# Kernel tuning notes

Measured on AMD Instinct MI355X. Metric: run time of the kernel, lower is better.

Reference implementation:

```python
import jax, jax.numpy as jnp
import numpy as np
from math import sqrt

N_PATCHES = 128
ATTENTION_WINDOW = 10
NEG_FILL = -10000.0


def _mask(L):
    # pid[i] = patch index of position i; channels = L // n_patches
    channels = L // N_PATCHES
    pid = jnp.repeat(jnp.arange(N_PATCHES), channels)
    diff = pid[None, :] - pid[:, None]  # diff[i, j] = pid[j] - pid[i]
    return (diff <= 0) | (diff >= ATTENTION_WINDOW)  # True = masked


def setup_inputs() -> dict:
    key = jax.random.key(0)
    k1, k2, k3 = jax.random.split(key, 3)
    B, H, L, D = 4, 8, 2048, 64
    return {
        "queries": jax.random.normal(k1, (B, H, L, D), dtype=jnp.float32),
        "keys": jax.random.normal(k2, (B, H, L, D), dtype=jnp.float32),
        "values": jax.random.normal(k3, (B, H, L, D), dtype=jnp.float32),
        "log_scale": jnp.asarray(np.log(2.0), dtype=jnp.float32),
    }


def reference(queries, keys, values, log_scale):
    B, H, L, D = queries.shape
    scores = jnp.einsum("bhqd,bhkd->bhqk", queries, keys)
    scale = jnp.clip(jnp.exp(log_scale), 1.0, 30.0) / sqrt(D)
    cmask = _mask(L)[None, None]  # [1,1,L,L]
    pos = jnp.where(cmask, NEG_FILL, scores)
    neg = jnp.where(cmask, NEG_FILL, -scores)
    A = jax.nn.softmax(scale * pos, axis=-1) - jax.nn.softmax(scale * neg, axis=-1)
    return jnp.einsum("bhqk,bhkd->bhqd", A, values)
```

## Files before the change

### kernel.cpp

```cpp
#include <hip/hip_runtime.h>
#include <hip/hip_bf16.h>


#define LSEQ   2048
#define DIM    64
#define CH     16
#define WIN    9
#define GRP    8
#define VCOLS  272

#define SK 72
#define SV 280
#define SA 168
#define UNELEMS 21504

typedef __attribute__((ext_vector_type(8))) short bf16x8;
typedef __attribute__((ext_vector_type(4))) float f32x4;

union BF8 { bf16x8 v; unsigned int u[4]; };

__device__ __forceinline__ unsigned int bfpack(float a, float b) {
  unsigned int ua = (__float_as_uint(a) + 0x8000u) >> 16;
  unsigned int ub = (__float_as_uint(b) + 0x8000u) & 0xFFFF0000u;
  return ua | ub;
}

__device__ __forceinline__ bf16x8 pack8(float4 a, float4 b) {
  BF8 r;
  r.u[0] = bfpack(a.x, a.y);
  r.u[1] = bfpack(a.z, a.w);
  r.u[2] = bfpack(b.x, b.y);
  r.u[3] = bfpack(b.z, b.w);
  return r.v;
}

__global__ __launch_bounds__(512, 4)
void signed_attn_kernel(const float* __restrict__ Q,
                        const float* __restrict__ K,
                        const float* __restrict__ V,
                        const float* __restrict__ LS,
                        float* __restrict__ O) {
  __shared__ __align__(16) unsigned short Vt[DIM * SV];
  __shared__ __align__(16) unsigned short Un[UNELEMS];

  const int g  = blockIdx.x & 15;
  const int bh = blockIdx.x >> 4;
  const int t  = threadIdx.x;
  const int p0 = g * GRP;

  const int kbp = (127 - p0) < 16 ? (127 - p0) : 16;
  const int kb  = kbp * CH;

  const float4* Kg = (const float4*)(K + ((size_t)bh * LSEQ + (size_t)(p0 + 1) * CH) * DIM);
  const float4* Vg = (const float4*)(V + ((size_t)bh * LSEQ + (size_t)(p0 + 1) * CH) * DIM);

  for (int e = t; e < kb * 16; e += 512) {
    int row = e >> 4, d4 = e & 15;
    float4 v = Kg[e];
    *(uint2*)&Un[row * SK + d4 * 4] = make_uint2(bfpack(v.x, v.y), bfpack(v.z, v.w));
  }
  {
    const int nq = kb >> 2;
    for (int e = t; e < nq * 16; e += 512) {
      int cq = e >> 4, d4 = e & 15;
      int c = cq << 2;
      float4 v0 = Vg[(c + 0) * 16 + d4];
      float4 v1 = Vg[(c + 1) * 16 + d4];
      float4 v2 = Vg[(c + 2) * 16 + d4];
      float4 v3 = Vg[(c + 3) * 16 + d4];
      int db = d4 << 2;
      *(uint2*)&Vt[(db + 0) * SV + c] = make_uint2(bfpack(v0.x, v1.x), bfpack(v2.x, v3.x));
      *(uint2*)&Vt[(db + 1) * SV + c] = make_uint2(bfpack(v0.y, v1.y), bfpack(v2.y, v3.y));
      *(uint2*)&Vt[(db + 2) * SV + c] = make_uint2(bfpack(v0.z, v1.z), bfpack(v2.z, v3.z));
      *(uint2*)&Vt[(db + 3) * SV + c] = make_uint2(bfpack(v0.w, v1.w), bfpack(v2.w, v3.w));
    }
  }
  for (int c = kb + (t >> 6); c < VCOLS; c += 8) Vt[(t & 63) * SV + c] = 0;

  const int w  = t >> 6;
  const int l  = t & 63;
  const int lr = l & 15;
  const int q4 = l >> 4;

  const int p   = p0 + w;
  const int npk = (127 - p) < WIN ? (127 - p) : WIN;

  const float* Qg = Q + ((size_t)bh * LSEQ + (size_t)p * CH) * DIM;
  bf16x8 qa[2];
#pragma unroll
  for (int s = 0; s < 2; s++) {
    const float* qp = Qg + lr * DIM + q4 * 8 + 32 * s;
    qa[s] = pack8(*(const float4*)qp, *(const float4*)(qp + 4));
  }

  const float scale = fminf(30.f, fmaxf(1.f, __expf(LS[0]))) * 0.125f;
  const int koff = w * CH;

  __syncthreads();

  f32x4 sacc[WIN];
#pragma unroll
  for (int tl = 0; tl < WIN; tl++) {
    f32x4 acc = {0.f, 0.f, 0.f, 0.f};
#pragma unroll
    for (int s = 0; s < 2; s++) {
      bf16x8 b = *(const bf16x8*)&Un[(koff + tl * 16 + lr) * SK + q4 * 8 + 32 * s];
      acc = __builtin_amdgcn_mfma_f32_16x16x32_bf16(qa[s], b, acc, 0, 0, 0);
    }
    sacc[tl] = acc;
  }

  __syncthreads();

  unsigned short* Aw = Un + w * 16 * SA;
#pragma unroll
  for (int tl = 0; tl < WIN; tl++) {
    const bool val = tl < npk;
#pragma unroll
    for (int r = 0; r < 4; r++) {
      float e1 = __expf(scale * sacc[tl][r]);
      unsigned int u = (__float_as_uint(e1) + 0x8000u) >> 16;
      Aw[(q4 * 4 + r) * SA + tl * 16 + lr] = (unsigned short)(val ? u : 0u);
    }
  }
#pragma unroll
  for (int r = 0; r < 4; r++)
    Aw[(q4 * 4 + r) * SA + 144 + lr] = 0;

  BF8 bones;
#pragma unroll
  for (int j = 0; j < 4; j++) bones.u[j] = 0x3F803F80u;

  f32x4 o1[4] = {{0,0,0,0},{0,0,0,0},{0,0,0,0},{0,0,0,0}};
  f32x4 o2[4] = {{0,0,0,0},{0,0,0,0},{0,0,0,0},{0,0,0,0}};
  f32x4 s1 = {0,0,0,0}, s2 = {0,0,0,0};

#pragma unroll
  for (int s = 0; s < 5; s++) {
    BF8 a1, a2;
    a1.v = *(const bf16x8*)&Aw[lr * SA + s * 32 + q4 * 8];
#pragma unroll
    for (int j = 0; j < 4; j++) {
      unsigned int d    = a1.u[j];
      unsigned int lo16 = d << 16;
      unsigned int hi16 = d & 0xFFFF0000u;
      float lo = __uint_as_float(lo16);
      float hi = __uint_as_float(hi16);
      float rl = (lo16 == 0u) ? 0.f : __builtin_amdgcn_rcpf(lo);
      float rh = (hi16 == 0u) ? 0.f : __builtin_amdgcn_rcpf(hi);
      a2.u[j] = bfpack(rl, rh);
    }
    s1 = __builtin_amdgcn_mfma_f32_16x16x32_bf16(a1.v, bones.v, s1, 0, 0, 0);
    s2 = __builtin_amdgcn_mfma_f32_16x16x32_bf16(a2.v, bones.v, s2, 0, 0, 0);
#pragma unroll
    for (int n = 0; n < 4; n++) {
      bf16x8 b = *(const bf16x8*)&Vt[(n * 16 + lr) * SV + koff + s * 32 + q4 * 8];
      o1[n] = __builtin_amdgcn_mfma_f32_16x16x32_bf16(a1.v, b, o1[n], 0, 0, 0);
      o2[n] = __builtin_amdgcn_mfma_f32_16x16x32_bf16(a2.v, b, o2[n], 0, 0, 0);
    }
  }

  float* Og = O + ((size_t)bh * LSEQ + (size_t)p * CH) * DIM;
  const bool live = (npk > 0);
#pragma unroll
  for (int r = 0; r < 4; r++) {
    float rp = __builtin_amdgcn_rcpf(s1[r]);
    float rn = __builtin_amdgcn_rcpf(s2[r]);
#pragma unroll
    for (int n = 0; n < 4; n++) {
      float o = o1[n][r] * rp - o2[n][r] * rn;
      Og[(q4 * 4 + r) * DIM + n * 16 + lr] = live ? o : 0.f;
    }
  }
}

extern "C" void kernel_launch(void* const* d_in, const int* in_sizes, int n_in,
                              void* d_out, int out_size, void* d_ws, size_t ws_size,
                              hipStream_t stream) {
  const float* Q  = (const float*)d_in[0];
  const float* K  = (const float*)d_in[1];
  const float* V  = (const float*)d_in[2];
  const float* LS = (const float*)d_in[3];
  float* O = (float*)d_out;
  signed_attn_kernel<<<dim3(512), dim3(512), 0, stream>>>(Q, K, V, LS, O);
}
```

Baseline: 102.0 us.

## Prepack K/V to bf16 in workspace and DMA tiles directly into LDS

Adds a separate prepack kernel that converts K to padded bf16 rows and V to a transposed bf16 layout in the workspace. The attention kernel then fills its LDS tiles with global_load_lds 16-byte DMA copies instead of per-thread fp32 loads, conversion and transposed stores. This is meant to remove in-kernel conversion work and cut the bytes each block fetches. In exchange it adds a second launch plus a full write and re-read of the packed K/V. Tail blocks also read past each head's valid range, relying on zeroed attention weights to cancel the extra values.

New measurement: 110.2 us. +8.0%, slower.

```diff
diff --git a/kernel.cpp b/kernel.cpp
--- a/kernel.cpp
+++ b/kernel.cpp
@@ -3,11 +3,9 @@
 
 
 #define LSEQ   2048
-#define DIM    64
 #define CH     16
 #define WIN    9
 #define GRP    8
-#define VCOLS  272
 
 #define SK 72
 #define SV 280
@@ -34,13 +32,51 @@
   return r.v;
 }
 
+__device__ __forceinline__ void dma16(const void* g, void* l) {
+  __builtin_amdgcn_global_load_lds(
+      (const __attribute__((address_space(1))) unsigned int*)g,
+      (__attribute__((address_space(3))) unsigned int*)l, 16, 0, 0);
+}
+
+__global__ __launch_bounds__(256)
+void prepack_kernel(const float* __restrict__ K, const float* __restrict__ V,
+                    unsigned short* __restrict__ Kp, unsigned short* __restrict__ Vp) {
+  int gidx = blockIdx.x * 256 + threadIdx.x;
+  if (gidx < 589824) {
+    int g   = gidx % 9;
+    int row = gidx / 9;
+    uint4 out;
+    if (g < 8) {
+      const float4* src = (const float4*)K + (size_t)row * 16 + 2 * g;
+      float4 a = src[0], b = src[1];
+      out = make_uint4(bfpack(a.x, a.y), bfpack(a.z, a.w),
+                       bfpack(b.x, b.y), bfpack(b.z, b.w));
+    } else {
+      out = make_uint4(0, 0, 0, 0);
+    }
+    *(uint4*)(Kp + (size_t)row * SK + g * 8) = out;
+  } else {
+    int vidx = gidx - 589824;
+    int d  = vidx & 63;
+    int cg = (vidx >> 6) & 255;
+    int bh = vidx >> 14;
+    const float* src = V + ((size_t)bh * LSEQ + cg * 8) * 64 + d;
+    float v[8];
+#pragma unroll
+    for (int j = 0; j < 8; j++) v[j] = src[j * 64];
+    uint4 out = make_uint4(bfpack(v[0], v[1]), bfpack(v[2], v[3]),
+                           bfpack(v[4], v[5]), bfpack(v[6], v[7]));
+    *(uint4*)(Vp + ((size_t)bh * 64 + d) * LSEQ + cg * 8) = out;
+  }
+}
+
 __global__ __launch_bounds__(512, 4)
 void signed_attn_kernel(const float* __restrict__ Q,
-                        const float* __restrict__ K,
-                        const float* __restrict__ V,
                         const float* __restrict__ LS,
+                        const unsigned short* __restrict__ Kp,
+                        const unsigned short* __restrict__ Vp,
                         float* __restrict__ O) {
-  __shared__ __align__(16) unsigned short Vt[DIM * SV];
+  __shared__ __align__(16) unsigned short Vt[64 * SV];
   __shared__ __align__(16) unsigned short Un[UNELEMS];
 
   const int g  = blockIdx.x & 15;
@@ -48,35 +84,6 @@
   const int t  = threadIdx.x;
   const int p0 = g * GRP;
 
-  const int kbp = (127 - p0) < 16 ? (127 - p0) : 16;
-  const int kb  = kbp * CH;
-
-  const float4* Kg = (const float4*)(K + ((size_t)bh * LSEQ + (size_t)(p0 + 1) * CH) * DIM);
-  const float4* Vg = (const float4*)(V + ((size_t)bh * LSEQ + (size_t)(p0 + 1) * CH) * DIM);
-
-  for (int e = t; e < kb * 16; e += 512) {
-    int row = e >> 4, d4 = e & 15;
-    float4 v = Kg[e];
-    *(uint2*)&Un[row * SK + d4 * 4] = make_uint2(bfpack(v.x, v.y), bfpack(v.z, v.w));
-  }
-  {
-    const int nq = kb >> 2;
-    for (int e = t; e < nq * 16; e += 512) {
-      int cq = e >> 4, d4 = e & 15;
-      int c = cq << 2;
-      float4 v0 = Vg[(c + 0) * 16 + d4];
-      float4 v1 = Vg[(c + 1) * 16 + d4];
-      float4 v2 = Vg[(c + 2) * 16 + d4];
-      float4 v3 = Vg[(c + 3) * 16 + d4];
-      int db = d4 << 2;
-      *(uint2*)&Vt[(db + 0) * SV + c] = make_uint2(bfpack(v0.x, v1.x), bfpack(v2.x, v3.x));
-      *(uint2*)&Vt[(db + 1) * SV + c] = make_uint2(bfpack(v0.y, v1.y), bfpack(v2.y, v3.y));
-      *(uint2*)&Vt[(db + 2) * SV + c] = make_uint2(bfpack(v0.z, v1.z), bfpack(v2.z, v3.z));
-      *(uint2*)&Vt[(db + 3) * SV + c] = make_uint2(bfpack(v0.w, v1.w), bfpack(v2.w, v3.w));
-    }
-  }
-  for (int c = kb + (t >> 6); c < VCOLS; c += 8) Vt[(t & 63) * SV + c] = 0;
-
   const int w  = t >> 6;
   const int l  = t & 63;
   const int lr = l & 15;
@@ -84,12 +91,27 @@
 
   const int p   = p0 + w;
   const int npk = (127 - p) < WIN ? (127 - p) : WIN;
-
-  const float* Qg = Q + ((size_t)bh * LSEQ + (size_t)p * CH) * DIM;
+  const int c0  = (p0 + 1) * CH;
+
+  const unsigned short* Kw = Kp + ((size_t)bh * LSEQ + c0) * SK;
+  for (int c = w; c < 36; c += 8)
+    dma16((const char*)Kw + c * 1024 + l * 16, (char*)Un + c * 1024);
+
+  const unsigned short* Vw = Vp + (size_t)bh * 64 * LSEQ + c0;
+  if (l < 32) {
+    for (int d = w; d < 64; d += 8)
+      dma16((const char*)(Vw + (size_t)d * LSEQ) + l * 16, (char*)Vt + d * (SV * 2));
+  }
+  for (int e = t; e < 64 * 12; e += 512) {
+    int d = e / 12, cdw = e % 12;
+    *(unsigned int*)((char*)Vt + d * (SV * 2) + 512 + cdw * 4) = 0u;
+  }
+
+  const float* Qg = Q + ((size_t)bh * LSEQ + (size_t)p * CH) * 64;
   bf16x8 qa[2];
 #pragma unroll
   for (int s = 0; s < 2; s++) {
-    const float* qp = Qg + lr * DIM + q4 * 8 + 32 * s;
+    const float* qp = Qg + lr * 64 + q4 * 8 + 32 * s;
     qa[s] = pack8(*(const float4*)qp, *(const float4*)(qp + 4));
   }
 
@@ -160,7 +182,7 @@
     }
   }
 
-  float* Og = O + ((size_t)bh * LSEQ + (size_t)p * CH) * DIM;
+  float* Og = O + ((size_t)bh * LSEQ + (size_t)p * CH) * 64;
   const bool live = (npk > 0);
 #pragma unroll
   for (int r = 0; r < 4; r++) {
@@ -169,7 +191,7 @@
 #pragma unroll
     for (int n = 0; n < 4; n++) {
       float o = o1[n][r] * rp - o2[n][r] * rn;
-      Og[(q4 * 4 + r) * DIM + n * 16 + lr] = live ? o : 0.f;
+      Og[(q4 * 4 + r) * 64 + n * 16 + lr] = live ? o : 0.f;
     }
   }
 }
@@ -182,5 +204,10 @@
   const float* V  = (const float*)d_in[2];
   const float* LS = (const float*)d_in[3];
   float* O = (float*)d_out;
-  signed_attn_kernel<<<dim3(512), dim3(512), 0, stream>>>(Q, K, V, LS, O);
-}
+
+  unsigned short* Kp = (unsigned short*)d_ws;
+  unsigned short* Vp = Kp + (size_t)32 * LSEQ * SK;
+
+  prepack_kernel<<<dim3(4352), dim3(256), 0, stream>>>(K, V, Kp, Vp);
+  signed_attn_kernel<<<dim3(512), dim3(512), 0, stream>>>(Q, LS, Kp, Vp, O);
+}
```

## Use one wave per patch and read K/V straight from global memory

Applied to the files above, without the earlier changes.

Each 64-thread block now handles a single query patch, so the grid grows from 512 blocks to 4096. K and V are read directly from global memory and converted to bf16 in registers, replacing the shared-memory staging across 8 patches. This removes the cooperative load phase, the large LDS footprint and the block-wide barriers. In exchange, overlapping K/V windows are re-read by neighbouring blocks, so global traffic goes up. The V loads become scalar strided gathers instead of vectorised transposed LDS reads.

New measurement: 127.2 us. 1.25x slower.

```diff
diff --git a/kernel.cpp b/kernel.cpp
--- a/kernel.cpp
+++ b/kernel.cpp
@@ -2,17 +2,10 @@
 #include <hip/hip_bf16.h>
 
 
-#define LSEQ   2048
-#define DIM    64
-#define CH     16
-#define WIN    9
-#define GRP    8
-#define VCOLS  272
-
-#define SK 72
-#define SV 280
-#define SA 168
-#define UNELEMS 21504
+#define LSEQ 2048
+#define CH   16
+#define WIN  9
+#define SA   168
 
 typedef __attribute__((ext_vector_type(8))) short bf16x8;
 typedef __attribute__((ext_vector_type(4))) float f32x4;
@@ -34,98 +27,69 @@
   return r.v;
 }
 
-__global__ __launch_bounds__(512, 4)
+__global__ __launch_bounds__(64, 4)
 void signed_attn_kernel(const float* __restrict__ Q,
                         const float* __restrict__ K,
                         const float* __restrict__ V,
                         const float* __restrict__ LS,
                         float* __restrict__ O) {
-  __shared__ __align__(16) unsigned short Vt[DIM * SV];
-  __shared__ __align__(16) unsigned short Un[UNELEMS];
+  __shared__ __align__(16) unsigned short As[16 * SA];
 
-  const int g  = blockIdx.x & 15;
-  const int bh = blockIdx.x >> 4;
-  const int t  = threadIdx.x;
-  const int p0 = g * GRP;
-
-  const int kbp = (127 - p0) < 16 ? (127 - p0) : 16;
-  const int kb  = kbp * CH;
-
-  const float4* Kg = (const float4*)(K + ((size_t)bh * LSEQ + (size_t)(p0 + 1) * CH) * DIM);
-  const float4* Vg = (const float4*)(V + ((size_t)bh * LSEQ + (size_t)(p0 + 1) * CH) * DIM);
-
-  for (int e = t; e < kb * 16; e += 512) {
-    int row = e >> 4, d4 = e & 15;
-    float4 v = Kg[e];
-    *(uint2*)&Un[row * SK + d4 * 4] = make_uint2(bfpack(v.x, v.y), bfpack(v.z, v.w));
-  }
-  {
-    const int nq = kb >> 2;
-    for (int e = t; e < nq * 16; e += 512) {
-      int cq = e >> 4, d4 = e & 15;
-      int c = cq << 2;
-      float4 v0 = Vg[(c + 0) * 16 + d4];
-      float4 v1 = Vg[(c + 1) * 16 + d4];
-      float4 v2 = Vg[(c + 2) * 16 + d4];
-      float4 v3 = Vg[(c + 3) * 16 + d4];
-      int db = d4 << 2;
-      *(uint2*)&Vt[(db + 0) * SV + c] = make_uint2(bfpack(v0.x, v1.x), bfpack(v2.x, v3.x));
-      *(uint2*)&Vt[(db + 1) * SV + c] = make_uint2(bfpack(v0.y, v1.y), bfpack(v2.y, v3.y));
-      *(uint2*)&Vt[(db + 2) * SV + c] = make_uint2(bfpack(v0.z, v1.z), bfpack(v2.z, v3.z));
-      *(uint2*)&Vt[(db + 3) * SV + c] = make_uint2(bfpack(v0.w, v1.w), bfpack(v2.w, v3.w));
-    }
-  }
-  for (int c = kb + (t >> 6); c < VCOLS; c += 8) Vt[(t & 63) * SV + c] = 0;
-
-  const int w  = t >> 6;
-  const int l  = t & 63;
+  const int p  = blockIdx.x & 127;
+  const int bh = blockIdx.x >> 7;
+  const int l  = threadIdx.x;
   const int lr = l & 15;
   const int q4 = l >> 4;
 
-  const int p   = p0 + w;
+  float* Og = O + ((size_t)bh * LSEQ + (size_t)p * CH) * 64;
   const int npk = (127 - p) < WIN ? (127 - p) : WIN;
 
-  const float* Qg = Q + ((size_t)bh * LSEQ + (size_t)p * CH) * DIM;
+  if (npk == 0) {
+#pragma unroll
+    for (int n = 0; n < 4; n++)
+#pragma unroll
+      for (int r = 0; r < 4; r++)
+        Og[(q4 * 4 + r) * 64 + n * 16 + lr] = 0.f;
+    return;
+  }
+
+  const int c0     = (p + 1) * CH;
+  const int maxoff = 2047 - c0;
+  const float scale = fminf(30.f, fmaxf(1.f, __expf(LS[0]))) * 0.125f;
+
+  const float* Qg = Q + ((size_t)bh * LSEQ + (size_t)p * CH) * 64;
   bf16x8 qa[2];
 #pragma unroll
   for (int s = 0; s < 2; s++) {
-    const float* qp = Qg + lr * DIM + q4 * 8 + 32 * s;
+    const float* qp = Qg + lr * 64 + q4 * 8 + 32 * s;
     qa[s] = pack8(*(const float4*)qp, *(const float4*)(qp + 4));
   }
 
-  const float scale = fminf(30.f, fmaxf(1.f, __expf(LS[0]))) * 0.125f;
-  const int koff = w * CH;
-
-  __syncthreads();
-
-  f32x4 sacc[WIN];
+  const float* Kb = K + ((size_t)bh * LSEQ + c0) * 64;
 #pragma unroll
   for (int tl = 0; tl < WIN; tl++) {
+    int ro = tl * 16 + lr;
+    ro = ro < maxoff ? ro : maxoff;
+    const float* kp = Kb + (size_t)ro * 64 + q4 * 8;
     f32x4 acc = {0.f, 0.f, 0.f, 0.f};
 #pragma unroll
     for (int s = 0; s < 2; s++) {
-      bf16x8 b = *(const bf16x8*)&Un[(koff + tl * 16 + lr) * SK + q4 * 8 + 32 * s];
+      bf16x8 b = pack8(*(const float4*)(kp + 32 * s), *(const float4*)(kp + 32 * s + 4));
       acc = __builtin_amdgcn_mfma_f32_16x16x32_bf16(qa[s], b, acc, 0, 0, 0);
     }
-    sacc[tl] = acc;
-  }
-
-  __syncthreads();
-
-  unsigned short* Aw = Un + w * 16 * SA;
-#pragma unroll
-  for (int tl = 0; tl < WIN; tl++) {
     const bool val = tl < npk;
 #pragma unroll
     for (int r = 0; r < 4; r++) {
-      float e1 = __expf(scale * sacc[tl][r]);
+      float e1 = __expf(scale * acc[r]);
       unsigned int u = (__float_as_uint(e1) + 0x8000u) >> 16;
-      Aw[(q4 * 4 + r) * SA + tl * 16 + lr] = (unsigned short)(val ? u : 0u);
+      As[(q4 * 4 + r) * SA + tl * 16 + lr] = (unsigned short)(val ? u : 0u);
     }
   }
 #pragma unroll
   for (int r = 0; r < 4; r++)
-    Aw[(q4 * 4 + r) * SA + 144 + lr] = 0;
+    As[(q4 * 4 + r) * SA + 144 + lr] = 0;
+
+  __syncthreads();
 
   BF8 bones;
 #pragma unroll
@@ -135,10 +99,11 @@
   f32x4 o2[4] = {{0,0,0,0},{0,0,0,0},{0,0,0,0},{0,0,0,0}};
   f32x4 s1 = {0,0,0,0}, s2 = {0,0,0,0};
 
+  const float* Vb = V + ((size_t)bh * LSEQ + c0) * 64;
 #pragma unroll
   for (int s = 0; s < 5; s++) {
     BF8 a1, a2;
-    a1.v = *(const bf16x8*)&Aw[lr * SA + s * 32 + q4 * 8];
+    a1.v = *(const bf16x8*)&As[lr * SA + s * 32 + q4 * 8];
 #pragma unroll
     for (int j = 0; j < 4; j++) {
       unsigned int d    = a1.u[j];
@@ -152,25 +117,35 @@
     }
     s1 = __builtin_amdgcn_mfma_f32_16x16x32_bf16(a1.v, bones.v, s1, 0, 0, 0);
     s2 = __builtin_amdgcn_mfma_f32_16x16x32_bf16(a2.v, bones.v, s2, 0, 0, 0);
+
+    int rof[8];
+#pragma unroll
+    for (int j = 0; j < 8; j++) {
+      int ro = s * 32 + q4 * 8 + j;
+      rof[j] = ro < maxoff ? ro : maxoff;
+    }
 #pragma unroll
     for (int n = 0; n < 4; n++) {
-      bf16x8 b = *(const bf16x8*)&Vt[(n * 16 + lr) * SV + koff + s * 32 + q4 * 8];
-      o1[n] = __builtin_amdgcn_mfma_f32_16x16x32_bf16(a1.v, b, o1[n], 0, 0, 0);
-      o2[n] = __builtin_amdgcn_mfma_f32_16x16x32_bf16(a2.v, b, o2[n], 0, 0, 0);
+      float v[8];
+#pragma unroll
+      for (int j = 0; j < 8; j++) v[j] = Vb[(size_t)rof[j] * 64 + n * 16 + lr];
+      BF8 b;
+      b.u[0] = bfpack(v[0], v[1]);
+      b.u[1] = bfpack(v[2], v[3]);
+      b.u[2] = bfpack(v[4], v[5]);
+      b.u[3] = bfpack(v[6], v[7]);
+      o1[n] = __builtin_amdgcn_mfma_f32_16x16x32_bf16(a1.v, b.v, o1[n], 0, 0, 0);
+      o2[n] = __builtin_amdgcn_mfma_f32_16x16x32_bf16(a2.v, b.v, o2[n], 0, 0, 0);
     }
   }
 
-  float* Og = O + ((size_t)bh * LSEQ + (size_t)p * CH) * DIM;
-  const bool live = (npk > 0);
 #pragma unroll
   for (int r = 0; r < 4; r++) {
     float rp = __builtin_amdgcn_rcpf(s1[r]);
     float rn = __builtin_amdgcn_rcpf(s2[r]);
 #pragma unroll
-    for (int n = 0; n < 4; n++) {
-      float o = o1[n][r] * rp - o2[n][r] * rn;
-      Og[(q4 * 4 + r) * DIM + n * 16 + lr] = live ? o : 0.f;
-    }
+    for (int n = 0; n < 4; n++)
+      Og[(q4 * 4 + r) * 64 + n * 16 + lr] = o1[n][r] * rp - o2[n][r] * rn;
   }
 }
 
@@ -182,5 +157,5 @@
   const float* V  = (const float*)d_in[2];
   const float* LS = (const float*)d_in[3];
   float* O = (float*)d_out;
-  signed_attn_kernel<<<dim3(512), dim3(512), 0, stream>>>(Q, K, V, LS, O);
+  signed_attn_kernel<<<dim3(4096), dim3(64), 0, stream>>>(Q, K, V, LS, O);
 }
```
